# Performance work log

Measured on AMD Instinct MI355X. Metric: run time of the kernel, lower is better.

## Reference

```python
import jax, jax.numpy as jnp
import numpy as np

N_HEADS, D_MODEL, D_HEAD, N_CTX = 16, 1024, 64, 2048
IGNORE = -100000.0


def setup_inputs() -> dict:
    key = jax.random.key(0)
    ks = jax.random.split(key, 8)
    B, S = 2, 2048
    return {
        "query_input": jax.random.normal(ks[0], (B, S, D_MODEL), jnp.float32),
        "key_input": jax.random.normal(ks[1], (B, S, D_MODEL), jnp.float32),
        "value_input": jax.random.normal(ks[2], (B, S, D_MODEL), jnp.float32),
        "additive_attention_mask": jnp.zeros((B, 1, 1, S), jnp.float32),
        "W_Q": jax.random.normal(ks[3], (N_HEADS, D_MODEL, D_HEAD), jnp.float32) * 0.02,
        "W_K": jax.random.normal(ks[4], (N_HEADS, D_MODEL, D_HEAD), jnp.float32) * 0.02,
        "W_V": jax.random.normal(ks[5], (N_HEADS, D_MODEL, D_HEAD), jnp.float32) * 0.02,
        "W_O": jax.random.normal(ks[6], (N_HEADS, D_HEAD, D_MODEL), jnp.float32) * 0.02,
        "b_Q": jnp.zeros((N_HEADS, D_HEAD), jnp.float32),
        "b_K": jnp.zeros((N_HEADS, D_HEAD), jnp.float32),
        "b_V": jnp.zeros((N_HEADS, D_HEAD), jnp.float32),
        "b_O": jnp.zeros((D_MODEL,), jnp.float32),
    }


def reference(query_input, key_input, value_input, additive_attention_mask,
              W_Q, W_K, W_V, W_O, b_Q, b_K, b_V, b_O):
    attn_scale = jnp.float32(np.sqrt(D_HEAD))
    # [batch, pos, head, d_head]
    q = jnp.einsum('bpm,hmd->bphd', query_input, W_Q) + b_Q
    k = jnp.einsum('bpm,hmd->bphd', key_input, W_K) + b_K
    v = jnp.einsum('bpm,hmd->bphd', value_input, W_V) + b_V
    # [batch, head, query_pos, key_pos]
    attn_scores = jnp.einsum('bqhd,bkhd->bhqk', q, k) / attn_scale
    S_q, S_k = attn_scores.shape[-2], attn_scores.shape[-1]
    causal = jnp.tril(jnp.ones((N_CTX, N_CTX), bool))[:S_q, :S_k]
    attn_scores = jnp.where(causal, attn_scores, jnp.float32(IGNORE))
    attn_scores = attn_scores + additive_attention_mask
    pattern = jax.nn.softmax(attn_scores, axis=-1)
    z = jnp.einsum('bkhd,bhqk->bqhd', v, pattern)
    out = jnp.einsum('bqhd,hdm->bqm', z, W_O) + b_O
    return out
```

## Files before the change

### kernel.cpp

```cpp
#include <hip/hip_runtime.h>
#include <hip/hip_bf16.h>

typedef __attribute__((ext_vector_type(8))) short s8;
typedef __attribute__((ext_vector_type(4))) short s4;
typedef __attribute__((ext_vector_type(4))) float f4;
typedef unsigned short u16;

__device__ __forceinline__ u16 f2bf(float f){
  union { float f; unsigned int i; } v; v.f = f;
  unsigned int x = v.i;
  return (u16)((x + 0x7fffu + ((x >> 16) & 1u)) >> 16);
}
__device__ __forceinline__ unsigned pk2bf(float a, float b){
  __hip_bfloat162 h = __float22bfloat162_rn(float2{a, b});
  union { __hip_bfloat162 h; unsigned u; } c; c.h = h; return c.u;
}
__device__ __forceinline__ s8 ld8(const u16* p){
  return *reinterpret_cast<const s8*>(p);
}
__device__ __forceinline__ void async16(const u16* g, u16* l){
  __builtin_amdgcn_global_load_lds(
      (const __attribute__((address_space(1))) unsigned int*)(g),
      (__attribute__((address_space(3))) unsigned int*)(l),
      16, 0, 0);
}

#define MFMA16(a, b, c) __builtin_amdgcn_mfma_f32_16x16x32_bf16((a), (b), (c), 0, 0, 0)

__global__ __launch_bounds__(256) void prep(
    const float* __restrict__ wq, const float* __restrict__ wk, const float* __restrict__ wv,
    const float* __restrict__ wo,
    const float* __restrict__ x0, const float* __restrict__ x1, const float* __restrict__ x2,
    u16* __restrict__ Wt, u16* __restrict__ Wto, u16* __restrict__ Xb)
{
  __shared__ __align__(16) u16 tile[64 * 65];
  const int id = blockIdx.x, t = threadIdx.x;
  if (id < 768) {
    const int mat = id >> 8, rem = id & 255, h = rem >> 4, kt = rem & 15;
    const float* W = mat == 0 ? wq : (mat == 1 ? wk : wv);
    const float* src = W + (size_t)h * 65536;
    u16* dst = Wt + (size_t)mat * 1048576 + (size_t)h * 65536;
    const int k0 = kt * 64;
    #pragma unroll
    for (int i = 0; i < 16; ++i) {
      int idx = i * 256 + t, kr = idx >> 6, d = idx & 63;
      tile[kr * 65 + d] = f2bf(src[(size_t)(k0 + kr) * 64 + d]);
    }
    __syncthreads();
    #pragma unroll
    for (int i = 0; i < 16; ++i) {
      int idx = i * 256 + t, d = idx >> 6, kr = idx & 63;
      dst[(size_t)d * 1024 + k0 + kr] = tile[kr * 65 + d];
    }
  } else if (id < 1024) {
    const int j = id - 768, r0 = (j >> 4) * 64, c0 = (j & 15) * 64;
    #pragma unroll
    for (int i = 0; i < 16; ++i) {
      int idx = i * 256 + t, rr = idx >> 6, cc = idx & 63;
      tile[rr * 65 + cc] = f2bf(wo[(size_t)(r0 + rr) * 1024 + c0 + cc]);
    }
    __syncthreads();
    #pragma unroll
    for (int i = 0; i < 16; ++i) {
      int idx = i * 256 + t, cc = idx >> 6, rr = idx & 63;
      Wto[(size_t)(c0 + cc) * 1024 + r0 + rr] = tile[rr * 65 + cc];
    }
  } else {
    const int j = id - 1024, m = j >> 11, xi = j & 2047;
    const float* src = m == 0 ? x0 : (m == 1 ? x1 : x2);
    u16* d = Xb + (size_t)m * 4194304;
    const size_t i = ((size_t)xi * 256 + t) * 8;
    const float4 a = *reinterpret_cast<const float4*>(src + i);
    const float4 b = *reinterpret_cast<const float4*>(src + i + 4);
    s8 o;
    o[0] = (short)f2bf(a.x); o[1] = (short)f2bf(a.y);
    o[2] = (short)f2bf(a.z); o[3] = (short)f2bf(a.w);
    o[4] = (short)f2bf(b.x); o[5] = (short)f2bf(b.y);
    o[6] = (short)f2bf(b.z); o[7] = (short)f2bf(b.w);
    *reinterpret_cast<s8*>(d + i) = o;
  }
}

#define GEMM_CORE(Aptr, Bptr)                                                  \
  f4 acc[4][4] = {};                                                           \
  {                                                                            \
    const int sr8 = lane >> 3;                                                 \
    const int sblk = (lane & 7) ^ sr8;                                         \
    const u16* pa = (Aptr) + (size_t)(wave * 32 + sr8) * 1024 + sblk * 8;      \
    const u16* pb = (Bptr) + (size_t)(wave * 32 + sr8) * 1024 + sblk * 8;      \
    u16* la = &AL[wave * 2048];                                                \
    u16* lb = &BL[wave * 2048];                                                \
    const int e = lm & 7;                                                      \
    for (int k0 = 0; k0 < 1024; k0 += 64) {                                    \
      _Pragma("unroll")                                                        \
      for (int j = 0; j < 4; ++j) {                                            \
        async16(pa + (size_t)j * 8192 + k0, la + j * 512);                     \
        async16(pb + (size_t)j * 8192 + k0, lb + j * 512);                     \
      }                                                                        \
      __syncthreads();                                                         \
      _Pragma("unroll")                                                        \
      for (int kb = 0; kb < 2; ++kb) {                                         \
        s8 af[4], bf[4];                                                       \
        _Pragma("unroll")                                                      \
        for (int i = 0; i < 4; ++i) {                                          \
          af[i] = ld8(&AL[(wm + i * 16 + lm) * 64 + (((kb * 4 + quad) ^ e) * 8)]); \
          bf[i] = ld8(&BL[(wn + i * 16 + lm) * 64 + (((kb * 4 + quad) ^ e) * 8)]); \
        }                                                                      \
        _Pragma("unroll")                                                      \
        for (int mt = 0; mt < 4; ++mt)                                         \
          _Pragma("unroll")                                                    \
          for (int nt = 0; nt < 4; ++nt)                                       \
            acc[mt][nt] = MFMA16(af[mt], bf[nt], acc[mt][nt]);                 \
      }                                                                        \
      __syncthreads();                                                         \
    }                                                                          \
  }

__global__ __launch_bounds__(256, 2) void qkv_gemm(
    const u16* __restrict__ Xb, const u16* __restrict__ Wt,
    const float* __restrict__ bq, const float* __restrict__ bk, const float* __restrict__ bv,
    u16* __restrict__ Qo, u16* __restrict__ Ko, u16* __restrict__ Vto)
{
  __shared__ __align__(16) u16 AL[128 * 64];
  __shared__ __align__(16) u16 BL[128 * 64];
  const int tM = blockIdx.x, tN = blockIdx.y;
  const int proj = (tN * 128) >> 10;
  const u16* A = Xb + (size_t)proj * 4194304 + (size_t)tM * 131072;
  const u16* B = Wt + (size_t)tN * 131072;
  const int t = threadIdx.x, wave = t >> 6, lane = t & 63;
  const int lm = lane & 15, quad = lane >> 4;
  const int wm = (wave & 1) * 64, wn = (wave >> 1) * 64;
  GEMM_CORE(A, B)
  const int mb = tM * 128 + wm;
  const int nb = tN * 128 + wn;
  if (proj < 2) {
    u16* O = proj == 0 ? Qo : Ko;
    const float* bi = proj == 0 ? bq : bk;
    #pragma unroll
    for (int nt = 0; nt < 4; ++nt) {
      const int nl = (nb + nt * 16 + lm) & 1023;
      const int h = nl >> 6, d = nl & 63;
      const float bb = bi[nl];
      #pragma unroll
      for (int mt = 0; mt < 4; ++mt) {
        const int m = mb + mt * 16 + quad * 4;
        const size_t base = ((size_t)((m >> 11) * 16 + h) * 2048 + (m & 2047)) * 64 + d;
        #pragma unroll
        for (int r = 0; r < 4; ++r)
          O[base + (size_t)r * 64] = f2bf(acc[mt][nt][r] + bb);
      }
    }
  } else {
    #pragma unroll
    for (int nt = 0; nt < 4; ++nt) {
      const int nl = (nb + nt * 16 + lm) & 1023;
      const int h = nl >> 6, d = nl & 63;
      const float bb = bv[nl];
      #pragma unroll
      for (int mt = 0; mt < 4; ++mt) {
        const int m = mb + mt * 16 + quad * 4;
        s4 pk;
        #pragma unroll
        for (int r = 0; r < 4; ++r) pk[r] = (short)f2bf(acc[mt][nt][r] + bb);
        *reinterpret_cast<s4*>(
            Vto + ((size_t)((m >> 11) * 16 + h) * 64 + d) * 2048 + (m & 2047)) = pk;
      }
    }
  }
}

__global__ __launch_bounds__(256, 2) void out_gemm(
    const u16* __restrict__ Zi, const u16* __restrict__ Wto,
    const float* __restrict__ bO, float* __restrict__ Out)
{
  __shared__ __align__(16) u16 AL[128 * 64];
  __shared__ __align__(16) u16 BL[128 * 64];
  const int tM = blockIdx.x, tN = blockIdx.y;
  const u16* A = Zi + (size_t)tM * 131072;
  const u16* B = Wto + (size_t)tN * 131072;
  const int t = threadIdx.x, wave = t >> 6, lane = t & 63;
  const int lm = lane & 15, quad = lane >> 4;
  const int wm = (wave & 1) * 64, wn = (wave >> 1) * 64;
  GEMM_CORE(A, B)
  const int mb = tM * 128 + wm;
  const int nb = tN * 128 + wn;
  #pragma unroll
  for (int nt = 0; nt < 4; ++nt) {
    const int n = nb + nt * 16 + lm;
    const float bb = bO[n];
    #pragma unroll
    for (int mt = 0; mt < 4; ++mt) {
      const int m = mb + mt * 16 + quad * 4;
      #pragma unroll
      for (int r = 0; r < 4; ++r)
        Out[(size_t)(m + r) * 1024 + n] = acc[mt][nt][r] + bb;
    }
  }
}

__global__ __launch_bounds__(256, 4) void attn(
    const u16* __restrict__ Q, const u16* __restrict__ K, const u16* __restrict__ Vt,
    const float* __restrict__ amask, u16* __restrict__ Z)
{
  __shared__ __align__(16) u16 KL[2][4096];
  __shared__ __align__(16) u16 VL[2][4096];
  __shared__ __align__(16) u16 Pl[4][1024];
  const int wg  = blockIdx.x;
  const int xcd = wg & 7, idx = wg >> 3;
  const int qi  = idx >> 2, bhl = idx & 3;
  const int qc  = 31 - qi;
  const int bh  = xcd * 4 + bhl;
  const int b   = bh >> 4, h = bh & 15;
  const int t = threadIdx.x, wave = t >> 6, lane = t & 63;
  const int lm = lane & 15, quad = lane >> 4;
  const u16* Qb = Q + (size_t)bh * 131072;
  const u16* Kb = K + (size_t)bh * 131072;
  const u16* Vb = Vt + (size_t)bh * 131072;
  const float* mk = amask + b * 2048;
  u16* Pw = Pl[wave];
  const int qw0 = qc * 64 + wave * 16;
  const int q = qw0 + lm;
  const s8 bQ0 = ld8(Qb + (size_t)q * 64 + quad * 8);
  const s8 bQ1 = ld8(Qb + (size_t)q * 64 + 32 + quad * 8);

  const int lr = lane >> 3;
  const int sw = (lane & 7) ^ lr;
  const int c0 = 2 * wave;
  const u16* pK0 = Kb + (c0 * 8 + lr) * 64 + sw * 8;
  const u16* pK1 = pK0 + 512;
  const u16* pV0 = Vb + (size_t)(c0 * 8 + lr) * 2048 + sw * 8;
  const u16* pV1 = pV0 + 8 * 2048;
  const int ldso = c0 * 512;

  const int e = lm & 7;
  const int fb0 = lm * 64 + ((quad ^ e) * 8);
  const int fb1 = lm * 64 + (((4 + quad) ^ e) * 8);

  f4 o[4] = {f4{0,0,0,0}, f4{0,0,0,0}, f4{0,0,0,0}, f4{0,0,0,0}};
  float psum = 0.f;
  const int nT = qc + 1;
  const float SC = 0.125f * 1.44269504f;

  async16(pK0, &KL[0][ldso]);       async16(pK1, &KL[0][ldso + 512]);
  async16(pV0, &VL[0][ldso]);       async16(pV1, &VL[0][ldso + 512]);
  pK0 += 4096; pK1 += 4096; pV0 += 64; pV1 += 64;

  for (int kt = 0; kt < nT; ++kt) {
    __syncthreads();
    if (kt + 1 < nT) {
      const int nb2 = (kt + 1) & 1;
      async16(pK0, &KL[nb2][ldso]);  async16(pK1, &KL[nb2][ldso + 512]);
      async16(pV0, &VL[nb2][ldso]);  async16(pV1, &VL[nb2][ldso + 512]);
      pK0 += 4096; pK1 += 4096; pV0 += 64; pV1 += 64;
    }
    const u16* Kc = KL[kt & 1];
    const u16* Vc = VL[kt & 1];
    const int k0 = kt * 64;
    f4 sc[4] = {f4{0,0,0,0}, f4{0,0,0,0}, f4{0,0,0,0}, f4{0,0,0,0}};
    #pragma unroll
    for (int nt = 0; nt < 4; ++nt) {
      sc[nt] = MFMA16(ld8(Kc + fb0 + nt * 1024), bQ0, sc[nt]);
      sc[nt] = MFMA16(ld8(Kc + fb1 + nt * 1024), bQ1, sc[nt]);
    }
    const bool masked = (kt == nT - 1);
    #pragma unroll
    for (int nt = 0; nt < 4; ++nt) {
      const int key0 = k0 + nt * 16 + quad * 4;
      const float4 mv = *reinterpret_cast<const float4*>(mk + key0);
      float p[4];
      if (masked) {
        #pragma unroll
        for (int r = 0; r < 4; ++r) {
          float s = (key0 + r <= q)
                    ? sc[nt][r] * SC + (&mv.x)[r] * 1.44269504f
                    : -__builtin_inff();
          p[r] = exp2f(s);
        }
      } else {
        #pragma unroll
        for (int r = 0; r < 4; ++r)
          p[r] = exp2f(sc[nt][r] * SC + (&mv.x)[r] * 1.44269504f);
      }
      psum += (p[0] + p[1]) + (p[2] + p[3]);
      const int wblk = (nt * 2 + (quad >> 1)) ^ e;
      *reinterpret_cast<uint2*>(&Pw[lm * 64 + wblk * 8 + (quad & 1) * 4]) =
          uint2{pk2bf(p[0], p[1]), pk2bf(p[2], p[3])};
    }
    __asm__ volatile("" ::: "memory");
    #pragma unroll
    for (int kb = 0; kb < 2; ++kb) {
      const int rblk = (kb * 4 + quad) ^ e;
      s8 bP = ld8(&Pw[lm * 64 + rblk * 8]);
      const int fb = kb ? fb1 : fb0;
      #pragma unroll
      for (int nt = 0; nt < 4; ++nt)
        o[nt] = MFMA16(ld8(Vc + fb + nt * 1024), bP, o[nt]);
    }
    __asm__ volatile("" ::: "memory");
  }

  psum += __shfl_xor(psum, 16, 64);
  psum += __shfl_xor(psum, 32, 64);
  const float inv = 1.0f / psum;
  u16* zr = Z + (size_t)(b * 2048 + q) * 1024 + h * 64;
  #pragma unroll
  for (int nt = 0; nt < 4; ++nt) {
    s4 pk;
    #pragma unroll
    for (int r = 0; r < 4; ++r) pk[r] = (short)f2bf(o[nt][r] * inv);
    *reinterpret_cast<s4*>(zr + nt * 16 + quad * 4) = pk;
  }
}

extern "C" void kernel_launch(void* const* d_in, const int* in_sizes, int n_in,
                              void* d_out, int out_size, void* d_ws, size_t ws_size,
                              hipStream_t stream)
{
  const float* xq = (const float*)d_in[0];
  const float* xk = (const float*)d_in[1];
  const float* xv = (const float*)d_in[2];
  const float* am = (const float*)d_in[3];
  const float* wq = (const float*)d_in[4];
  const float* wk = (const float*)d_in[5];
  const float* wv = (const float*)d_in[6];
  const float* wo = (const float*)d_in[7];
  const float* bq = (const float*)d_in[8];
  const float* bk = (const float*)d_in[9];
  const float* bv = (const float*)d_in[10];
  const float* bo = (const float*)d_in[11];
  u16* ws = (u16*)d_ws;
  const size_t M1 = 1u << 20;
  u16* Wt  = ws;
  u16* Wto = ws + 3 * M1;
  u16* Xb  = ws + 4 * M1;
  u16* Qw  = ws + 16 * M1;
  u16* Kw  = ws + 20 * M1;
  u16* Vtw = ws + 24 * M1;
  u16* Zw  = ws + 28 * M1;

  prep<<<dim3(7168), 256, 0, stream>>>(wq, wk, wv, wo, xq, xk, xv, Wt, Wto, Xb);
  qkv_gemm<<<dim3(32, 24), 256, 0, stream>>>(Xb, Wt, bq, bk, bv, Qw, Kw, Vtw);
  attn<<<dim3(1024), 256, 0, stream>>>(Qw, Kw, Vtw, am, Zw);
  out_gemm<<<dim3(32, 8), 256, 0, stream>>>(Zw, Wto, bo, (float*)d_out);
}
```

Before: 222.1 us.

## Pair causal query chunks per block and process 128-key tiles per barrier

Each attention block now handles two query chunks (qc and 31-qc) so causal work per block is balanced, and the grid is halved. The K/V tiles grow to 128 keys per double-buffered stage, which halves the number of barriers and async-load rounds per key. A separate tail path handles an odd tile count. The larger shared-memory footprint lowers the occupancy target from 4 to 2 blocks per CU, which can cost latency hiding.

```diff
diff --git a/kernel.cpp b/kernel.cpp
--- a/kernel.cpp
+++ b/kernel.cpp
@@ -198,117 +198,165 @@
   }
 }
 
-__global__ __launch_bounds__(256, 4) void attn(
+__device__ __forceinline__ void qk_scores(const u16* Kc, s8 bQ0, s8 bQ1,
+                                          int fb0, int fb1, f4 sc[4])
+{
+  #pragma unroll
+  for (int nt = 0; nt < 4; ++nt) {
+    sc[nt] = MFMA16(ld8(Kc + fb0 + nt * 1024), bQ0, sc[nt]);
+    sc[nt] = MFMA16(ld8(Kc + fb1 + nt * 1024), bQ1, sc[nt]);
+  }
+}
+
+__device__ __forceinline__ float softmax_p(const f4 sc[4], int k0, bool masked,
+                                           int q, const float* __restrict__ mk,
+                                           u16* Pp, int lm, int quad, int e)
+{
+  const float SC = 0.125f * 1.44269504f;
+  float psum = 0.f;
+  #pragma unroll
+  for (int nt = 0; nt < 4; ++nt) {
+    const int key0 = k0 + nt * 16 + quad * 4;
+    const float4 mv = *reinterpret_cast<const float4*>(mk + key0);
+    float p[4];
+    if (masked) {
+      #pragma unroll
+      for (int r = 0; r < 4; ++r) {
+        float s = (key0 + r <= q)
+                  ? sc[nt][r] * SC + (&mv.x)[r] * 1.44269504f
+                  : -__builtin_inff();
+        p[r] = exp2f(s);
+      }
+    } else {
+      #pragma unroll
+      for (int r = 0; r < 4; ++r)
+        p[r] = exp2f(sc[nt][r] * SC + (&mv.x)[r] * 1.44269504f);
+    }
+    psum += (p[0] + p[1]) + (p[2] + p[3]);
+    const int wblk = (nt * 2 + (quad >> 1)) ^ e;
+    *reinterpret_cast<uint2*>(&Pp[lm * 64 + wblk * 8 + (quad & 1) * 4]) =
+        uint2{pk2bf(p[0], p[1]), pk2bf(p[2], p[3])};
+  }
+  return psum;
+}
+
+__device__ __forceinline__ void pv_acc(const u16* Vc, const u16* Pp,
+                                       int fb0, int fb1, int lm, int quad,
+                                       int e, f4 o[4])
+{
+  #pragma unroll
+  for (int kb = 0; kb < 2; ++kb) {
+    const int rblk = (kb * 4 + quad) ^ e;
+    s8 bP = ld8(&Pp[lm * 64 + rblk * 8]);
+    const int fb = kb ? fb1 : fb0;
+    #pragma unroll
+    for (int nt = 0; nt < 4; ++nt)
+      o[nt] = MFMA16(ld8(Vc + fb + nt * 1024), bP, o[nt]);
+  }
+}
+
+__global__ __launch_bounds__(256, 2) void attn(
     const u16* __restrict__ Q, const u16* __restrict__ K, const u16* __restrict__ Vt,
     const float* __restrict__ amask, u16* __restrict__ Z)
 {
-  __shared__ __align__(16) u16 KL[2][4096];
-  __shared__ __align__(16) u16 VL[2][4096];
-  __shared__ __align__(16) u16 Pl[4][1024];
-  const int wg  = blockIdx.x;
-  const int xcd = wg & 7, idx = wg >> 3;
-  const int qi  = idx >> 2, bhl = idx & 3;
-  const int qc  = 31 - qi;
-  const int bh  = xcd * 4 + bhl;
-  const int b   = bh >> 4, h = bh & 15;
+  __shared__ __align__(16) u16 KL[2][8192];
+  __shared__ __align__(16) u16 VL[2][8192];
+  __shared__ __align__(16) u16 Pl[4][2048];
+  const int wg   = blockIdx.x;
+  const int xcd  = wg & 7, rest = wg >> 3;
+  const int bhl  = rest & 3, j = rest >> 2;
+  const int bh   = xcd * 4 + bhl;
+  const int b    = bh >> 4, h = bh & 15;
   const int t = threadIdx.x, wave = t >> 6, lane = t & 63;
   const int lm = lane & 15, quad = lane >> 4;
   const u16* Qb = Q + (size_t)bh * 131072;
   const u16* Kb = K + (size_t)bh * 131072;
   const u16* Vb = Vt + (size_t)bh * 131072;
   const float* mk = amask + b * 2048;
-  u16* Pw = Pl[wave];
-  const int qw0 = qc * 64 + wave * 16;
-  const int q = qw0 + lm;
-  const s8 bQ0 = ld8(Qb + (size_t)q * 64 + quad * 8);
-  const s8 bQ1 = ld8(Qb + (size_t)q * 64 + 32 + quad * 8);
+  u16* PwA = Pl[wave];
+  u16* PwB = Pl[wave] + 1024;
 
   const int lr = lane >> 3;
   const int sw = (lane & 7) ^ lr;
-  const int c0 = 2 * wave;
-  const u16* pK0 = Kb + (c0 * 8 + lr) * 64 + sw * 8;
-  const u16* pK1 = pK0 + 512;
-  const u16* pV0 = Vb + (size_t)(c0 * 8 + lr) * 2048 + sw * 8;
-  const u16* pV1 = pV0 + 8 * 2048;
-  const int ldso = c0 * 512;
-
   const int e = lm & 7;
   const int fb0 = lm * 64 + ((quad ^ e) * 8);
   const int fb1 = lm * 64 + (((4 + quad) ^ e) * 8);
 
-  f4 o[4] = {f4{0,0,0,0}, f4{0,0,0,0}, f4{0,0,0,0}, f4{0,0,0,0}};
-  float psum = 0.f;
-  const int nT = qc + 1;
-  const float SC = 0.125f * 1.44269504f;
-
-  async16(pK0, &KL[0][ldso]);       async16(pK1, &KL[0][ldso + 512]);
-  async16(pV0, &VL[0][ldso]);       async16(pV1, &VL[0][ldso + 512]);
-  pK0 += 4096; pK1 += 4096; pV0 += 64; pV1 += 64;
-
-  for (int kt = 0; kt < nT; ++kt) {
+  #pragma unroll 1
+  for (int half = 0; half < 2; ++half) {
+    const int qc = half == 0 ? 31 - j : j;
+    const int nT = qc + 1, nFull = nT >> 1, nPairs = (nT + 1) >> 1;
+    const int q = qc * 64 + wave * 16 + lm;
+    const s8 bQ0 = ld8(Qb + (size_t)q * 64 + quad * 8);
+    const s8 bQ1 = ld8(Qb + (size_t)q * 64 + 32 + quad * 8);
+    f4 o[4] = {f4{0,0,0,0}, f4{0,0,0,0}, f4{0,0,0,0}, f4{0,0,0,0}};
+    float psum = 0.f;
+
     __syncthreads();
-    if (kt + 1 < nT) {
-      const int nb2 = (kt + 1) & 1;
-      async16(pK0, &KL[nb2][ldso]);  async16(pK1, &KL[nb2][ldso + 512]);
-      async16(pV0, &VL[nb2][ldso]);  async16(pV1, &VL[nb2][ldso + 512]);
-      pK0 += 4096; pK1 += 4096; pV0 += 64; pV1 += 64;
-    }
-    const u16* Kc = KL[kt & 1];
-    const u16* Vc = VL[kt & 1];
-    const int k0 = kt * 64;
-    f4 sc[4] = {f4{0,0,0,0}, f4{0,0,0,0}, f4{0,0,0,0}, f4{0,0,0,0}};
+    {
+      const u16* gk = Kb + (size_t)(16 * wave + lr) * 64 + sw * 8;
+      u16* kd = KL[0] + 1024 * wave;
+      async16(gk, kd);                async16(gk + 512, kd + 512);
+      async16(gk + 4096, kd + 4096);  async16(gk + 4608, kd + 4608);
+      const u16* gv = Vb + (size_t)(16 * wave + lr) * 2048 + sw * 8;
+      u16* vd = VL[0] + 1024 * wave;
+      async16(gv, vd);                 async16(gv + 16384, vd + 512);
+      async16(gv + 64, vd + 4096);     async16(gv + 16448, vd + 4608);
+    }
+
+    for (int it = 0; it < nFull; ++it) {
+      __syncthreads();
+      if (it + 1 < nPairs) {
+        const int p2 = (it + 1) & 1;
+        const int kb0 = (it + 1) * 128;
+        const u16* gk = Kb + (size_t)(kb0 + 16 * wave + lr) * 64 + sw * 8;
+        u16* kd = KL[p2] + 1024 * wave;
+        async16(gk, kd);                async16(gk + 512, kd + 512);
+        async16(gk + 4096, kd + 4096);  async16(gk + 4608, kd + 4608);
+        const u16* gv = Vb + (size_t)(16 * wave + lr) * 2048 + kb0 + sw * 8;
+        u16* vd = VL[p2] + 1024 * wave;
+        async16(gv, vd);                 async16(gv + 16384, vd + 512);
+        async16(gv + 64, vd + 4096);     async16(gv + 16448, vd + 4608);
+      }
+      const u16* Kc = KL[it & 1];
+      const u16* Vc = VL[it & 1];
+      const int k0 = it * 128;
+      const bool mB = (it == nFull - 1) && !(nT & 1);
+      f4 s0[4] = {f4{0,0,0,0}, f4{0,0,0,0}, f4{0,0,0,0}, f4{0,0,0,0}};
+      f4 s1[4] = {f4{0,0,0,0}, f4{0,0,0,0}, f4{0,0,0,0}, f4{0,0,0,0}};
+      qk_scores(Kc,        bQ0, bQ1, fb0, fb1, s0);
+      qk_scores(Kc + 4096, bQ0, bQ1, fb0, fb1, s1);
+      psum += softmax_p(s0, k0,      false, q, mk, PwA, lm, quad, e);
+      psum += softmax_p(s1, k0 + 64, mB,    q, mk, PwB, lm, quad, e);
+      __asm__ volatile("" ::: "memory");
+      pv_acc(Vc,        PwA, fb0, fb1, lm, quad, e, o);
+      pv_acc(Vc + 4096, PwB, fb0, fb1, lm, quad, e, o);
+      __asm__ volatile("" ::: "memory");
+    }
+    if (nT & 1) {
+      __syncthreads();
+      const u16* Kc = KL[nFull & 1];
+      const u16* Vc = VL[nFull & 1];
+      const int k0 = nFull * 128;
+      f4 s0[4] = {f4{0,0,0,0}, f4{0,0,0,0}, f4{0,0,0,0}, f4{0,0,0,0}};
+      qk_scores(Kc, bQ0, bQ1, fb0, fb1, s0);
+      psum += softmax_p(s0, k0, true, q, mk, PwA, lm, quad, e);
+      __asm__ volatile("" ::: "memory");
+      pv_acc(Vc, PwA, fb0, fb1, lm, quad, e, o);
+      __asm__ volatile("" ::: "memory");
+    }
+
+    psum += __shfl_xor(psum, 16, 64);
+    psum += __shfl_xor(psum, 32, 64);
+    const float inv = 1.0f / psum;
+    u16* zr = Z + (size_t)(b * 2048 + q) * 1024 + h * 64;
     #pragma unroll
     for (int nt = 0; nt < 4; ++nt) {
-      sc[nt] = MFMA16(ld8(Kc + fb0 + nt * 1024), bQ0, sc[nt]);
-      sc[nt] = MFMA16(ld8(Kc + fb1 + nt * 1024), bQ1, sc[nt]);
-    }
-    const bool masked = (kt == nT - 1);
-    #pragma unroll
-    for (int nt = 0; nt < 4; ++nt) {
-      const int key0 = k0 + nt * 16 + quad * 4;
-      const float4 mv = *reinterpret_cast<const float4*>(mk + key0);
-      float p[4];
-      if (masked) {
-        #pragma unroll
-        for (int r = 0; r < 4; ++r) {
-          float s = (key0 + r <= q)
-                    ? sc[nt][r] * SC + (&mv.x)[r] * 1.44269504f
-                    : -__builtin_inff();
-          p[r] = exp2f(s);
-        }
-      } else {
-        #pragma unroll
-        for (int r = 0; r < 4; ++r)
-          p[r] = exp2f(sc[nt][r] * SC + (&mv.x)[r] * 1.44269504f);
-      }
-      psum += (p[0] + p[1]) + (p[2] + p[3]);
-      const int wblk = (nt * 2 + (quad >> 1)) ^ e;
-      *reinterpret_cast<uint2*>(&Pw[lm * 64 + wblk * 8 + (quad & 1) * 4]) =
-          uint2{pk2bf(p[0], p[1]), pk2bf(p[2], p[3])};
-    }
-    __asm__ volatile("" ::: "memory");
-    #pragma unroll
-    for (int kb = 0; kb < 2; ++kb) {
-      const int rblk = (kb * 4 + quad) ^ e;
-      s8 bP = ld8(&Pw[lm * 64 + rblk * 8]);
-      const int fb = kb ? fb1 : fb0;
-      #pragma unroll
-      for (int nt = 0; nt < 4; ++nt)
-        o[nt] = MFMA16(ld8(Vc + fb + nt * 1024), bP, o[nt]);
-    }
-    __asm__ volatile("" ::: "memory");
-  }
-
-  psum += __shfl_xor(psum, 16, 64);
-  psum += __shfl_xor(psum, 32, 64);
-  const float inv = 1.0f / psum;
-  u16* zr = Z + (size_t)(b * 2048 + q) * 1024 + h * 64;
-  #pragma unroll
-  for (int nt = 0; nt < 4; ++nt) {
-    s4 pk;
-    #pragma unroll
-    for (int r = 0; r < 4; ++r) pk[r] = (short)f2bf(o[nt][r] * inv);
-    *reinterpret_cast<s4*>(zr + nt * 16 + quad * 4) = pk;
+      s4 pk;
+      #pragma unroll
+      for (int r = 0; r < 4; ++r) pk[r] = (short)f2bf(o[nt][r] * inv);
+      *reinterpret_cast<s4*>(zr + nt * 16 + quad * 4) = pk;
+    }
   }
 }
 
@@ -340,6 +388,6 @@
 
   prep<<<dim3(7168), 256, 0, stream>>>(wq, wk, wv, wo, xq, xk, xv, Wt, Wto, Xb);
   qkv_gemm<<<dim3(32, 24), 256, 0, stream>>>(Xb, Wt, bq, bk, bv, Qw, Kw, Vtw);
-  attn<<<dim3(1024), 256, 0, stream>>>(Qw, Kw, Vtw, am, Zw);
+  attn<<<dim3(512), 256, 0, stream>>>(Qw, Kw, Vtw, am, Zw);
   out_gemm<<<dim3(32, 8), 256, 0, stream>>>(Zw, Wto, bo, (float*)d_out);
 }
```

New measurement: 226.6 us. 1.02x slower.

## Process 128-query tiles per attention block, two query rows per wave

Applied to the files above, without the earlier changes.

The attention kernel now covers 128 queries per workgroup, with each wave handling two 16-row query sub-tiles. Each K/V fragment loaded from LDS is reused for both sub-tiles, and half as many blocks each load the K/V tiles. Waves whose diagonal tile has already passed skip compute while still helping with the loads, and the block order alternates long and short causal rows to balance work. GEMM launch bounds are raised to 3 blocks per CU and attention drops to 2. The cost is more registers per wave, idle waves on the diagonal tiles, and a grid of only 512 blocks.

```diff
diff --git a/kernel.cpp b/kernel.cpp
--- a/kernel.cpp
+++ b/kernel.cpp
@@ -116,7 +116,7 @@
     }                                                                          \
   }
 
-__global__ __launch_bounds__(256, 2) void qkv_gemm(
+__global__ __launch_bounds__(256, 3) void qkv_gemm(
     const u16* __restrict__ Xb, const u16* __restrict__ Wt,
     const float* __restrict__ bq, const float* __restrict__ bk, const float* __restrict__ bv,
     u16* __restrict__ Qo, u16* __restrict__ Ko, u16* __restrict__ Vto)
@@ -169,7 +169,7 @@
   }
 }
 
-__global__ __launch_bounds__(256, 2) void out_gemm(
+__global__ __launch_bounds__(256, 3) void out_gemm(
     const u16* __restrict__ Zi, const u16* __restrict__ Wto,
     const float* __restrict__ bO, float* __restrict__ Out)
 {
@@ -198,17 +198,49 @@
   }
 }
 
-__global__ __launch_bounds__(256, 4) void attn(
+__device__ __forceinline__ float softmax_p(const f4 sc[4], int k0, bool masked,
+                                           int q, const float* __restrict__ mk,
+                                           u16* Pp, int lm, int quad, int e)
+{
+  const float SC = 0.125f * 1.44269504f;
+  float psum = 0.f;
+  #pragma unroll
+  for (int nt = 0; nt < 4; ++nt) {
+    const int key0 = k0 + nt * 16 + quad * 4;
+    const float4 mv = *reinterpret_cast<const float4*>(mk + key0);
+    float p[4];
+    if (masked) {
+      #pragma unroll
+      for (int r = 0; r < 4; ++r) {
+        float s = (key0 + r <= q)
+                  ? sc[nt][r] * SC + (&mv.x)[r] * 1.44269504f
+                  : -__builtin_inff();
+        p[r] = exp2f(s);
+      }
+    } else {
+      #pragma unroll
+      for (int r = 0; r < 4; ++r)
+        p[r] = exp2f(sc[nt][r] * SC + (&mv.x)[r] * 1.44269504f);
+    }
+    psum += (p[0] + p[1]) + (p[2] + p[3]);
+    const int wblk = (nt * 2 + (quad >> 1)) ^ e;
+    *reinterpret_cast<uint2*>(&Pp[lm * 64 + wblk * 8 + (quad & 1) * 4]) =
+        uint2{pk2bf(p[0], p[1]), pk2bf(p[2], p[3])};
+  }
+  return psum;
+}
+
+__global__ __launch_bounds__(256, 2) void attn(
     const u16* __restrict__ Q, const u16* __restrict__ K, const u16* __restrict__ Vt,
     const float* __restrict__ amask, u16* __restrict__ Z)
 {
   __shared__ __align__(16) u16 KL[2][4096];
   __shared__ __align__(16) u16 VL[2][4096];
-  __shared__ __align__(16) u16 Pl[4][1024];
+  __shared__ __align__(16) u16 Pl[4][2048];
   const int wg  = blockIdx.x;
-  const int xcd = wg & 7, idx = wg >> 3;
-  const int qi  = idx >> 2, bhl = idx & 3;
-  const int qc  = 31 - qi;
+  const int xcd = wg & 7, rest = wg >> 3;
+  const int bhl = rest & 3, idx = rest >> 2;
+  const int c   = (idx & 1) ? (idx >> 1) : 15 - (idx >> 1);
   const int bh  = xcd * 4 + bhl;
   const int b   = bh >> 4, h = bh & 15;
   const int t = threadIdx.x, wave = t >> 6, lane = t & 63;
@@ -217,98 +249,96 @@
   const u16* Kb = K + (size_t)bh * 131072;
   const u16* Vb = Vt + (size_t)bh * 131072;
   const float* mk = amask + b * 2048;
-  u16* Pw = Pl[wave];
-  const int qw0 = qc * 64 + wave * 16;
-  const int q = qw0 + lm;
-  const s8 bQ0 = ld8(Qb + (size_t)q * 64 + quad * 8);
-  const s8 bQ1 = ld8(Qb + (size_t)q * 64 + 32 + quad * 8);
+  u16* PwA = Pl[wave];
+  u16* PwB = Pl[wave] + 1024;
 
   const int lr = lane >> 3;
-  const int sw = (lane & 7) ^ lr;
-  const int c0 = 2 * wave;
-  const u16* pK0 = Kb + (c0 * 8 + lr) * 64 + sw * 8;
-  const u16* pK1 = pK0 + 512;
-  const u16* pV0 = Vb + (size_t)(c0 * 8 + lr) * 2048 + sw * 8;
-  const u16* pV1 = pV0 + 8 * 2048;
-  const int ldso = c0 * 512;
-
+  const int sw8 = ((lane & 7) ^ lr) * 8;
   const int e = lm & 7;
   const int fb0 = lm * 64 + ((quad ^ e) * 8);
   const int fb1 = lm * 64 + (((4 + quad) ^ e) * 8);
 
-  f4 o[4] = {f4{0,0,0,0}, f4{0,0,0,0}, f4{0,0,0,0}, f4{0,0,0,0}};
-  float psum = 0.f;
-  const int nT = qc + 1;
-  const float SC = 0.125f * 1.44269504f;
-
-  async16(pK0, &KL[0][ldso]);       async16(pK1, &KL[0][ldso + 512]);
-  async16(pV0, &VL[0][ldso]);       async16(pV1, &VL[0][ldso + 512]);
-  pK0 += 4096; pK1 += 4096; pV0 += 64; pV1 += 64;
+  const int nT  = 2 * c + 2;
+  const int mkt = 2 * c + (wave >> 1);
+  const int qA  = c * 128 + wave * 32 + lm;
+  const int qB  = qA + 16;
+  const s8 bQA0 = ld8(Qb + (size_t)qA * 64 + quad * 8);
+  const s8 bQA1 = ld8(Qb + (size_t)qA * 64 + 32 + quad * 8);
+  const s8 bQB0 = ld8(Qb + (size_t)qB * 64 + quad * 8);
+  const s8 bQB1 = ld8(Qb + (size_t)qB * 64 + 32 + quad * 8);
+  f4 oA[4] = {f4{0,0,0,0}, f4{0,0,0,0}, f4{0,0,0,0}, f4{0,0,0,0}};
+  f4 oB[4] = {f4{0,0,0,0}, f4{0,0,0,0}, f4{0,0,0,0}, f4{0,0,0,0}};
+  float psA = 0.f, psB = 0.f;
+
+  const int sK = 1024 * wave;
+  {
+    const u16* gk = Kb + (size_t)(16 * wave + lr) * 64 + sw8;
+    async16(gk, KL[0] + sK);          async16(gk + 512, KL[0] + sK + 512);
+    const u16* gv = Vb + (size_t)(16 * wave + lr) * 2048 + sw8;
+    async16(gv, VL[0] + sK);          async16(gv + 16384, VL[0] + sK + 512);
+  }
 
   for (int kt = 0; kt < nT; ++kt) {
     __syncthreads();
     if (kt + 1 < nT) {
-      const int nb2 = (kt + 1) & 1;
-      async16(pK0, &KL[nb2][ldso]);  async16(pK1, &KL[nb2][ldso + 512]);
-      async16(pV0, &VL[nb2][ldso]);  async16(pV1, &VL[nb2][ldso + 512]);
-      pK0 += 4096; pK1 += 4096; pV0 += 64; pV1 += 64;
-    }
-    const u16* Kc = KL[kt & 1];
-    const u16* Vc = VL[kt & 1];
-    const int k0 = kt * 64;
-    f4 sc[4] = {f4{0,0,0,0}, f4{0,0,0,0}, f4{0,0,0,0}, f4{0,0,0,0}};
-    #pragma unroll
-    for (int nt = 0; nt < 4; ++nt) {
-      sc[nt] = MFMA16(ld8(Kc + fb0 + nt * 1024), bQ0, sc[nt]);
-      sc[nt] = MFMA16(ld8(Kc + fb1 + nt * 1024), bQ1, sc[nt]);
-    }
-    const bool masked = (kt == nT - 1);
-    #pragma unroll
-    for (int nt = 0; nt < 4; ++nt) {
-      const int key0 = k0 + nt * 16 + quad * 4;
-      const float4 mv = *reinterpret_cast<const float4*>(mk + key0);
-      float p[4];
-      if (masked) {
+      const int bf2 = (kt + 1) & 1;
+      const int k1 = (kt + 1) * 64;
+      const u16* gk = Kb + (size_t)(k1 + 16 * wave + lr) * 64 + sw8;
+      async16(gk, KL[bf2] + sK);       async16(gk + 512, KL[bf2] + sK + 512);
+      const u16* gv = Vb + (size_t)(16 * wave + lr) * 2048 + k1 + sw8;
+      async16(gv, VL[bf2] + sK);       async16(gv + 16384, VL[bf2] + sK + 512);
+    }
+    if (kt <= mkt) {
+      const u16* Kc = KL[kt & 1];
+      const u16* Vc = VL[kt & 1];
+      const int k0 = kt * 64;
+      f4 sA[4] = {f4{0,0,0,0}, f4{0,0,0,0}, f4{0,0,0,0}, f4{0,0,0,0}};
+      f4 sB[4] = {f4{0,0,0,0}, f4{0,0,0,0}, f4{0,0,0,0}, f4{0,0,0,0}};
+      #pragma unroll
+      for (int nt = 0; nt < 4; ++nt) {
+        const s8 kf0 = ld8(Kc + fb0 + nt * 1024);
+        const s8 kf1 = ld8(Kc + fb1 + nt * 1024);
+        sA[nt] = MFMA16(kf0, bQA0, sA[nt]);
+        sA[nt] = MFMA16(kf1, bQA1, sA[nt]);
+        sB[nt] = MFMA16(kf0, bQB0, sB[nt]);
+        sB[nt] = MFMA16(kf1, bQB1, sB[nt]);
+      }
+      const bool masked = (kt == mkt);
+      psA += softmax_p(sA, k0, masked, qA, mk, PwA, lm, quad, e);
+      psB += softmax_p(sB, k0, masked, qB, mk, PwB, lm, quad, e);
+      __asm__ volatile("" ::: "memory");
+      #pragma unroll
+      for (int kb = 0; kb < 2; ++kb) {
+        const int rblk = (kb * 4 + quad) ^ e;
+        const s8 bPA = ld8(PwA + lm * 64 + rblk * 8);
+        const s8 bPB = ld8(PwB + lm * 64 + rblk * 8);
+        const int fb = kb ? fb1 : fb0;
         #pragma unroll
-        for (int r = 0; r < 4; ++r) {
-          float s = (key0 + r <= q)
-                    ? sc[nt][r] * SC + (&mv.x)[r] * 1.44269504f
-                    : -__builtin_inff();
-          p[r] = exp2f(s);
+        for (int nt = 0; nt < 4; ++nt) {
+          const s8 vf = ld8(Vc + fb + nt * 1024);
+          oA[nt] = MFMA16(vf, bPA, oA[nt]);
+          oB[nt] = MFMA16(vf, bPB, oB[nt]);
         }
-      } else {
-        #pragma unroll
-        for (int r = 0; r < 4; ++r)
-          p[r] = exp2f(sc[nt][r] * SC + (&mv.x)[r] * 1.44269504f);
-      }
-      psum += (p[0] + p[1]) + (p[2] + p[3]);
-      const int wblk = (nt * 2 + (quad >> 1)) ^ e;
-      *reinterpret_cast<uint2*>(&Pw[lm * 64 + wblk * 8 + (quad & 1) * 4]) =
-          uint2{pk2bf(p[0], p[1]), pk2bf(p[2], p[3])};
-    }
-    __asm__ volatile("" ::: "memory");
-    #pragma unroll
-    for (int kb = 0; kb < 2; ++kb) {
-      const int rblk = (kb * 4 + quad) ^ e;
-      s8 bP = ld8(&Pw[lm * 64 + rblk * 8]);
-      const int fb = kb ? fb1 : fb0;
-      #pragma unroll
-      for (int nt = 0; nt < 4; ++nt)
-        o[nt] = MFMA16(ld8(Vc + fb + nt * 1024), bP, o[nt]);
-    }
-    __asm__ volatile("" ::: "memory");
-  }
-
-  psum += __shfl_xor(psum, 16, 64);
-  psum += __shfl_xor(psum, 32, 64);
-  const float inv = 1.0f / psum;
-  u16* zr = Z + (size_t)(b * 2048 + q) * 1024 + h * 64;
+      }
+      __asm__ volatile("" ::: "memory");
+    }
+  }
+
+  psA += __shfl_xor(psA, 16, 64);  psA += __shfl_xor(psA, 32, 64);
+  psB += __shfl_xor(psB, 16, 64);  psB += __shfl_xor(psB, 32, 64);
+  const float invA = 1.0f / psA, invB = 1.0f / psB;
+  u16* zrA = Z + (size_t)(b * 2048 + qA) * 1024 + h * 64;
+  u16* zrB = Z + (size_t)(b * 2048 + qB) * 1024 + h * 64;
   #pragma unroll
   for (int nt = 0; nt < 4; ++nt) {
-    s4 pk;
-    #pragma unroll
-    for (int r = 0; r < 4; ++r) pk[r] = (short)f2bf(o[nt][r] * inv);
-    *reinterpret_cast<s4*>(zr + nt * 16 + quad * 4) = pk;
+    s4 pkA, pkB;
+    #pragma unroll
+    for (int r = 0; r < 4; ++r) {
+      pkA[r] = (short)f2bf(oA[nt][r] * invA);
+      pkB[r] = (short)f2bf(oB[nt][r] * invB);
+    }
+    *reinterpret_cast<s4*>(zrA + nt * 16 + quad * 4) = pkA;
+    *reinterpret_cast<s4*>(zrB + nt * 16 + quad * 4) = pkB;
   }
 }
 
@@ -340,6 +370,6 @@
 
   prep<<<dim3(7168), 256, 0, stream>>>(wq, wk, wv, wo, xq, xk, xv, Wt, Wto, Xb);
   qkv_gemm<<<dim3(32, 24), 256, 0, stream>>>(Xb, Wt, bq, bk, bv, Qw, Kw, Vtw);
-  attn<<<dim3(1024), 256, 0, stream>>>(Qw, Kw, Vtw, am, Zw);
+  attn<<<dim3(512), 256, 0, stream>>>(Qw, Kw, Vtw, am, Zw);
   out_gemm<<<dim3(32, 8), 256, 0, stream>>>(Zw, Wto, bo, (float*)d_out);
 }
```

Result: slower. 260.8 us (+17.4%).
